# Kernel optimization log

Hardware: AMD Instinct MI355X
Metric: run time of the kernel (lower is better)

The kernel has to match this reference:

```python
import jax, jax.numpy as jnp
import numpy as np

N_NODES = 100000
N_EDGES = 600000
D = 128
N_TYPES = 3


def setup_inputs() -> dict:
    key = jax.random.key(0)
    ks = jax.random.split(key, 10)
    x = jax.random.normal(ks[0], (N_NODES, D), dtype=jnp.float32)
    edge_index = jax.random.randint(ks[1], (2, N_EDGES), 0, N_NODES, dtype=jnp.int64)
    edge_type_ids = jax.random.randint(ks[2], (N_EDGES,), 0, N_TYPES, dtype=jnp.int32)
    edge_weights = jax.random.uniform(ks[3], (N_EDGES,), dtype=jnp.float32)
    # Xavier-uniform linear weights (in==out==D), zero biases, uniform attention
    limit = float(np.sqrt(6.0 / (D + D)))
    W_edge = jax.random.uniform(ks[4], (N_TYPES, D, D), minval=-limit, maxval=limit, dtype=jnp.float32)
    b_edge = jnp.zeros((N_TYPES, D), dtype=jnp.float32)
    W_self = jax.random.uniform(ks[5], (D, D), minval=-limit, maxval=limit, dtype=jnp.float32)
    b_self = jnp.zeros((D,), dtype=jnp.float32)
    attention = jnp.ones((N_TYPES + 1,), dtype=jnp.float32) / (N_TYPES + 1)
    return {"x": x, "edge_index": edge_index, "edge_type_ids": edge_type_ids,
            "edge_weights": edge_weights, "W_edge": W_edge, "b_edge": b_edge,
            "W_self": W_self, "b_self": b_self, "attention": attention}


def reference(x, edge_index, edge_type_ids, edge_weights, W_edge, b_edge, W_self, b_self, attention):
    n_nodes = x.shape[0]
    n_types = W_edge.shape[0]
    src, dst = edge_index[0], edge_index[1]
    xs = x[src]  # (E, D) gather once, shared by all edge types
    outs = []
    for t in range(n_types):  # small fixed set of structurally distinct linears
        # mask zeros out edges of other types; equivalent to torch's boolean slicing
        m = jnp.where(edge_type_ids == t, edge_weights, jnp.zeros((), x.dtype))
        y = (xs @ W_edge[t] + b_edge[t]) * m[:, None]  # (E, D)
        outs.append(jax.ops.segment_sum(y, dst, num_segments=n_nodes))  # scatter-add
    outs.append(x @ W_self + b_self)
    stacked = jnp.stack(outs, axis=-1)  # (N, D, n_types+1)
    attn = jax.nn.softmax(attention)
    out = jnp.sum(stacked * attn, axis=-1)
    return jax.nn.gelu(out, approximate=False)  # torch F.gelu default is erf-based
```

## Files before the change

kernel.cpp:

```cpp
#include <hip/hip_runtime.h>
#include <hip/hip_bf16.h>
#include <math.h>

#define D 128
#define NT 3
#define KTOT (D * (NT + 1))
#define TM 32

typedef __attribute__((ext_vector_type(8))) __bf16 bf16x8;
typedef __attribute__((ext_vector_type(4))) float f32x4;

__device__ inline unsigned short f2bf(float f) {
    unsigned int u = __float_as_uint(f);
    unsigned int r = (u + 0x7FFFu + ((u >> 16) & 1u)) >> 16;
    return (unsigned short)r;
}
__device__ inline float bf2f(unsigned int hi16_as_low) {
    return __uint_as_float(hi16_as_low << 16);
}

__global__ void zero_kernel(float* __restrict__ p, long long n4) {
    long long i = (long long)blockIdx.x * blockDim.x + threadIdx.x;
    long long stride = (long long)gridDim.x * blockDim.x;
    float4 z = make_float4(0.f, 0.f, 0.f, 0.f);
    for (; i < n4; i += stride) ((float4*)p)[i] = z;
}

__global__ void prep_kernel(const float* __restrict__ W_edge, const float* __restrict__ b_edge,
                            const float* __restrict__ W_self, const float* __restrict__ b_self,
                            const float* __restrict__ attention,
                            float* __restrict__ wcat, float* __restrict__ biasb,
                            unsigned short* __restrict__ bfrag,
                            int* __restrict__ deg, int degN) {
    float a0 = attention[0], a1 = attention[1], a2 = attention[2], a3 = attention[3];
    float m = fmaxf(fmaxf(a0, a1), fmaxf(a2, a3));
    float e0 = expf(a0 - m), e1 = expf(a1 - m), e2 = expf(a2 - m), e3 = expf(a3 - m);
    float inv = 1.f / (e0 + e1 + e2 + e3);
    float at[4] = {e0 * inv, e1 * inv, e2 * inv, e3 * inv};

    int idx0 = blockIdx.x * blockDim.x + threadIdx.x;
    int stride = gridDim.x * blockDim.x;
    if (deg) {
        for (int i = idx0; i < degN; i += stride) deg[i] = 0;
    }
    for (int i = idx0; i < KTOT * D; i += stride) {
        int k = i >> 7, j = i & (D - 1);
        float v;
        if (k < D) {
            v = at[NT] * W_self[k * D + j];
        } else {
            int t = (k - D) >> 7;
            int kk = (k - D) & (D - 1);
            v = at[t] * W_edge[(t * D + kk) * D + j];
        }
        wcat[i] = v;
    }
    for (int i = idx0; i < KTOT; i += stride) {
        if (i < NT * D) {
            int t = i >> 7, j = i & (D - 1);
            biasb[i] = at[t] * b_edge[t * D + j];
        } else {
            biasb[i] = at[NT] * b_self[i - NT * D];
        }
    }
    if (bfrag) {
        for (int i = idx0; i < 16 * 8 * 64; i += stride) {
            int l = i & 63;
            int cf = (i >> 6) & 7;
            int step = i >> 9;
            int col = cf * 16 + (l & 15);
            int kb = step * 32 + ((l >> 4) * 8);
#pragma unroll
            for (int j = 0; j < 8; ++j) {
                int k = kb + j;
                float v;
                if (k < D) {
                    v = at[NT] * W_self[k * D + col];
                } else {
                    int t = (k - D) >> 7;
                    int kk = (k - D) & (D - 1);
                    v = at[t] * W_edge[(t * D + kk) * D + col];
                }
                bfrag[(size_t)i * 8 + j] = f2bf(v);
            }
        }
    }
}

__global__ __launch_bounds__(256) void fill_kernel(
    const int* __restrict__ ei, const int* __restrict__ et, const float* __restrict__ ew,
    int* __restrict__ deg, int2* __restrict__ csr, int* __restrict__ ovfcnt,
    int* __restrict__ ovflist, int nE, int cap) {
    int e = blockIdx.x * blockDim.x + threadIdx.x;
    if (e >= nE) return;
    int dst = ei[nE + e];
    int pos = atomicAdd(deg + dst, 1);
    if (pos < cap) {
        int src = ei[e];
        int t = et[e];
        csr[(size_t)dst * cap + pos] = make_int2(src | (t << 20), __float_as_int(ew[e]));
    } else {
        int o = atomicAdd(ovfcnt, 1);
        ovflist[o] = e;
    }
}

__global__ __launch_bounds__(512, 6) void fused_gemm_kernel(
    const float* __restrict__ x, const int2* __restrict__ csr, const int* __restrict__ deg,
    const unsigned short* __restrict__ bfrag, const float* __restrict__ biasb,
    const int* __restrict__ ei, const int* __restrict__ et, const float* __restrict__ ew,
    const int* __restrict__ ovfc, const int* __restrict__ ovfl,
    float* __restrict__ out, int nN, int nE, int cap) {
    __shared__ unsigned char lds[49536];
    float* sL = (float*)(lds + 49152);
    int t = threadIdx.x;
    int w = t >> 6;
    int lane = t & 63;
    int gl = lane & 15;
    int gbase = lane & 48;
    int row0 = blockIdx.x * TM;

#define BSTAGE(buf, st_) do {                                                                     \
        const unsigned short* gsrc = bfrag + (size_t)(st_) * 4096 + w * 512 + lane * 8;           \
        unsigned char* ldst = lds + 32768 + (buf) * 8192 + w * 1024;                              \
        __builtin_amdgcn_global_load_lds((const __attribute__((address_space(1))) void*)gsrc,     \
                                         (__attribute__((address_space(3))) void*)ldst, 16, 0, 0);\
    } while (0)

    BSTAGE(0, 0);

    int lrow = w * 4 + (lane >> 4);
    int node = row0 + lrow;
    int nclamp = (node < nN) ? node : (nN - 1);
    int dg = (node < nN) ? deg[nclamp] : 0;
    if (dg > cap) dg = cap;
    const int2* c = csr + (size_t)nclamp * cap;
    int2 mA = (gl < dg) ? c[gl] : make_int2(0, 0);
    int2 mB = (gl + 16 < dg) ? c[gl + 16] : make_int2(0, 0);

    float ac0[8], ac1[8], ac2[8];
#pragma unroll
    for (int j = 0; j < 8; ++j) { ac0[j] = 0.f; ac1[j] = 0.f; ac2[j] = 0.f; }
    float sw0 = 0.f, sw1 = 0.f, sw2 = 0.f;

    for (int i = 0; i < dg; i += 2) {
        int slA = gbase + (i & 15);
        int exA = __shfl((i < 16) ? mA.x : mB.x, slA);
        int ewA = __shfl((i < 16) ? mA.y : mB.y, slA);
        int srcA = exA & 0xFFFFF;
        if (srcA >= nN) srcA = 0;
        float wA = __int_as_float(ewA);
        int tA = (exA >> 20) & 3;
        bool actB = (i + 1 < dg);
        int slB = gbase + ((i + 1) & 15);
        int exB = __shfl((i + 1 < 16) ? mA.x : mB.x, slB);
        int ewB = __shfl((i + 1 < 16) ? mA.y : mB.y, slB);
        int srcB = exB & 0xFFFFF;
        if (!actB || srcB >= nN) srcB = 0;
        float wB = actB ? __int_as_float(ewB) : 0.f;
        int tB = (exB >> 20) & 3;

        const float* xsA = x + (size_t)srcA * D + gl * 8;
        const float* xsB = x + (size_t)srcB * D + gl * 8;
        float4 a0 = *(const float4*)(xsA);
        float4 a1 = *(const float4*)(xsA + 4);
        float4 b0 = *(const float4*)(xsB);
        float4 b1 = *(const float4*)(xsB + 4);

        float wA0 = (tA == 0) ? wA : 0.f;
        float wA1 = (tA == 1) ? wA : 0.f;
        float wA2 = (tA == 2) ? wA : 0.f;
        float wB0 = (tB == 0) ? wB : 0.f;
        float wB1 = (tB == 1) ? wB : 0.f;
        float wB2 = (tB == 2) ? wB : 0.f;
        sw0 += wA0 + wB0; sw1 += wA1 + wB1; sw2 += wA2 + wB2;

#define ACC4(v, j0, wt0, wt1, wt2)                                         \
        ac0[j0+0] = fmaf(wt0, v.x, ac0[j0+0]); ac0[j0+1] = fmaf(wt0, v.y, ac0[j0+1]); \
        ac0[j0+2] = fmaf(wt0, v.z, ac0[j0+2]); ac0[j0+3] = fmaf(wt0, v.w, ac0[j0+3]); \
        ac1[j0+0] = fmaf(wt1, v.x, ac1[j0+0]); ac1[j0+1] = fmaf(wt1, v.y, ac1[j0+1]); \
        ac1[j0+2] = fmaf(wt1, v.z, ac1[j0+2]); ac1[j0+3] = fmaf(wt1, v.w, ac1[j0+3]); \
        ac2[j0+0] = fmaf(wt2, v.x, ac2[j0+0]); ac2[j0+1] = fmaf(wt2, v.y, ac2[j0+1]); \
        ac2[j0+2] = fmaf(wt2, v.z, ac2[j0+2]); ac2[j0+3] = fmaf(wt2, v.w, ac2[j0+3]);
        ACC4(a0, 0, wA0, wA1, wA2)
        ACC4(a1, 4, wA0, wA1, wA2)
        ACC4(b0, 0, wB0, wB1, wB2)
        ACC4(b1, 4, wB0, wB1, wB2)
#undef ACC4
    }

    {
        int swz = lrow & 15;
        const float* xo = x + (size_t)nclamp * D + gl * 8;
        float4 v0 = *(const float4*)(xo);
        float4 v1 = *(const float4*)(xo + 4);
        uint4 o;
        o.x = (unsigned int)f2bf(v0.x) | ((unsigned int)f2bf(v0.y) << 16);
        o.y = (unsigned int)f2bf(v0.z) | ((unsigned int)f2bf(v0.w) << 16);
        o.z = (unsigned int)f2bf(v1.x) | ((unsigned int)f2bf(v1.y) << 16);
        o.w = (unsigned int)f2bf(v1.z) | ((unsigned int)f2bf(v1.w) << 16);
        *(uint4*)(lds + lrow * 1024 + ((gl ^ swz) << 4)) = o;
#define PACKST(arr, tt)                                                                \
        o.x = (unsigned int)f2bf(arr[0]) | ((unsigned int)f2bf(arr[1]) << 16);         \
        o.y = (unsigned int)f2bf(arr[2]) | ((unsigned int)f2bf(arr[3]) << 16);         \
        o.z = (unsigned int)f2bf(arr[4]) | ((unsigned int)f2bf(arr[5]) << 16);         \
        o.w = (unsigned int)f2bf(arr[6]) | ((unsigned int)f2bf(arr[7]) << 16);         \
        *(uint4*)(lds + lrow * 1024 + 256 + (tt) * 256 + ((gl ^ swz) << 4)) = o;
        PACKST(ac0, 0)
        PACKST(ac1, 1)
        PACKST(ac2, 2)
#undef PACKST
        if (gl < 3) {
            float sv = (gl == 0) ? sw0 : ((gl == 1) ? sw1 : sw2);
            sL[lrow * NT + gl] = sv;
        }
    }
    __syncthreads();

    int cnt = *ovfc;
    if (cnt > 0) {
        if (w == 0 && lane < 16) {
            for (int i = 0; i < cnt; ++i) {
                int e = ovfl[i];
                int dst = ei[nE + e];
                if (dst >= row0 && dst < row0 + TM && dst < nN) {
                    int tt = et[e];
                    float wt = ew[e];
                    int src = ei[e];
                    int lr = dst - row0;
                    int swz = lr & 15;
                    uint4* p = (uint4*)(lds + lr * 1024 + 256 + tt * 256 + ((lane ^ swz) << 4));
                    uint4 cu = *p;
                    const float* xs = x + (size_t)src * D + lane * 8;
                    float4 q0 = *(const float4*)(xs);
                    float4 q1 = *(const float4*)(xs + 4);
                    float f[8];
                    f[0] = bf2f(cu.x & 0xFFFF) + wt * q0.x; f[1] = bf2f(cu.x >> 16) + wt * q0.y;
                    f[2] = bf2f(cu.y & 0xFFFF) + wt * q0.z; f[3] = bf2f(cu.y >> 16) + wt * q0.w;
                    f[4] = bf2f(cu.z & 0xFFFF) + wt * q1.x; f[5] = bf2f(cu.z >> 16) + wt * q1.y;
                    f[6] = bf2f(cu.w & 0xFFFF) + wt * q1.z; f[7] = bf2f(cu.w >> 16) + wt * q1.w;
                    cu.x = (unsigned int)f2bf(f[0]) | ((unsigned int)f2bf(f[1]) << 16);
                    cu.y = (unsigned int)f2bf(f[2]) | ((unsigned int)f2bf(f[3]) << 16);
                    cu.z = (unsigned int)f2bf(f[4]) | ((unsigned int)f2bf(f[5]) << 16);
                    cu.w = (unsigned int)f2bf(f[6]) | ((unsigned int)f2bf(f[7]) << 16);
                    *p = cu;
                    if (lane == 0) sL[lr * NT + tt] += wt;
                }
            }
        }
        __syncthreads();
    }

    int ll = lane & 15;
    int ck = lane >> 4;
    f32x4 acc0 = (f32x4){0.f, 0.f, 0.f, 0.f};
    f32x4 acc1 = (f32x4){0.f, 0.f, 0.f, 0.f};
#pragma unroll 2
    for (int st = 0; st < 16; ++st) {
        int cur = st & 1;
        if (st < 15) BSTAGE(cur ^ 1, st + 1);
        int cc = st * 4 + ck;
        int phys = (cc & 48) | ((cc & 15) ^ ll);
        bf16x8 a0 = *(const bf16x8*)(lds + ll * 1024 + (phys << 4));
        bf16x8 a1 = *(const bf16x8*)(lds + (16 + ll) * 1024 + (phys << 4));
        bf16x8 b = *(const bf16x8*)(lds + 32768 + cur * 8192 + ((w * 64 + lane) << 4));
        acc0 = __builtin_amdgcn_mfma_f32_16x16x32_bf16(a0, b, acc0, 0, 0, 0);
        acc1 = __builtin_amdgcn_mfma_f32_16x16x32_bf16(a1, b, acc1, 0, 0, 0);
        __syncthreads();
    }
#undef BSTAGE

    int colb = w * 16 + ll;
    float bb0 = biasb[colb], bb1 = biasb[D + colb], bb2 = biasb[2 * D + colb], bs4 = biasb[3 * D + colb];
    const float kInvSqrt2 = 0.70710678118654752440f;
#pragma unroll
    for (int fr = 0; fr < 2; ++fr) {
        f32x4 A = fr ? acc1 : acc0;
#pragma unroll
        for (int reg = 0; reg < 4; ++reg) {
            int lr = fr * 16 + ck * 4 + reg;
            long row = (long)row0 + lr;
            if (row >= nN) continue;
            float s0 = sL[lr * NT + 0];
            float s1 = sL[lr * NT + 1];
            float s2 = sL[lr * NT + 2];
            float v = A[reg] + bs4 + s0 * bb0 + s1 * bb1 + s2 * bb2;
            v = 0.5f * v * (1.f + erff(v * kInvSqrt2));
            out[row * D + colb] = v;
        }
    }
}

__global__ __launch_bounds__(256) void scatterA_kernel(
    const float* __restrict__ x, const int* __restrict__ ei,
    const int* __restrict__ et, const float* __restrict__ ew,
    float* __restrict__ agg, float* __restrict__ s, int nE) {
    int gtid = blockIdx.x * blockDim.x + threadIdx.x;
    int wave = gtid >> 6;
    int lane = threadIdx.x & 63;
    int nw = (gridDim.x * blockDim.x) >> 6;
    for (int e = wave; e < nE; e += nw) {
        int src = ei[e];
        int dst = ei[nE + e];
        int t = et[e];
        float w = ew[e];
        float2 xv = *(const float2*)(x + (size_t)src * D + lane * 2);
        float* p = agg + (size_t)dst * (NT * D) + t * D + lane * 2;
        unsafeAtomicAdd(p, w * xv.x);
        unsafeAtomicAdd(p + 1, w * xv.y);
        if (lane == 0) unsafeAtomicAdd(s + (size_t)dst * NT + t, w);
    }
}

#define BM 64
#define BK 32
__global__ __launch_bounds__(256) void gemm_gelu_kernel(
    const float* __restrict__ x, const float* __restrict__ agg,
    const float* __restrict__ s, const float* __restrict__ wcat,
    const float* __restrict__ biasb, float* __restrict__ out, int nNodes) {
    __shared__ float As[BK][BM + 1];
    __shared__ float Bs[BK][D];

    int tx = threadIdx.x;
    int row0 = blockIdx.x * BM;
    int cg = tx & 31;
    int rg = tx >> 5;
    int lr = tx >> 3;
    int lc = (tx & 7) * 4;

    float acc[8][4];
#pragma unroll
    for (int i = 0; i < 8; ++i)
#pragma unroll
        for (int j = 0; j < 4; ++j) acc[i][j] = 0.f;

    for (int k0 = 0; k0 < KTOT; k0 += BK) {
        const float* srcBase;
        int strideA, koff;
        if (k0 < D) { srcBase = x; strideA = D; koff = k0; }
        else        { srcBase = agg; strideA = NT * D; koff = k0 - D; }
#pragma unroll
        for (int h = 0; h < 2; ++h) {
            int r = lr + h * 32;
            int node = row0 + r;
            if (node >= nNodes) node = nNodes - 1;
            float4 v = *(const float4*)(srcBase + (size_t)node * strideA + koff + lc);
            As[lc + 0][r] = v.x; As[lc + 1][r] = v.y;
            As[lc + 2][r] = v.z; As[lc + 3][r] = v.w;
        }
        {
            int br = tx >> 5;
            int bc = (tx & 31) * 4;
#pragma unroll
            for (int h = 0; h < 4; ++h) {
                int r = br + h * 8;
                *(float4*)(&Bs[r][bc]) = *(const float4*)(wcat + (size_t)(k0 + r) * D + bc);
            }
        }
        __syncthreads();
#pragma unroll
        for (int kk = 0; kk < BK; ++kk) {
            float4 b = *(const float4*)(&Bs[kk][cg * 4]);
            float a[8];
            *(float4*)(a)     = *(const float4*)(&As[kk][rg * 8]);
            *(float4*)(a + 4) = *(const float4*)(&As[kk][rg * 8 + 4]);
#pragma unroll
            for (int i = 0; i < 8; ++i) {
                acc[i][0] = fmaf(a[i], b.x, acc[i][0]);
                acc[i][1] = fmaf(a[i], b.y, acc[i][1]);
                acc[i][2] = fmaf(a[i], b.z, acc[i][2]);
                acc[i][3] = fmaf(a[i], b.w, acc[i][3]);
            }
        }
        __syncthreads();
    }

    int jc = cg * 4;
    float4 bb0 = *(const float4*)(biasb + 0 * D + jc);
    float4 bb1 = *(const float4*)(biasb + 1 * D + jc);
    float4 bb2 = *(const float4*)(biasb + 2 * D + jc);
    float4 bsv = *(const float4*)(biasb + NT * D + jc);
#pragma unroll
    for (int i = 0; i < 8; ++i) {
        int node = row0 + rg * 8 + i;
        if (node >= nNodes) break;
        float s0 = s[(size_t)node * NT + 0];
        float s1 = s[(size_t)node * NT + 1];
        float s2 = s[(size_t)node * NT + 2];
        float4 r;
        r.x = acc[i][0] + bsv.x + s0 * bb0.x + s1 * bb1.x + s2 * bb2.x;
        r.y = acc[i][1] + bsv.y + s0 * bb0.y + s1 * bb1.y + s2 * bb2.y;
        r.z = acc[i][2] + bsv.z + s0 * bb0.z + s1 * bb1.z + s2 * bb2.z;
        r.w = acc[i][3] + bsv.w + s0 * bb0.w + s1 * bb1.w + s2 * bb2.w;
        const float kInvSqrt2 = 0.70710678118654752440f;
        r.x = 0.5f * r.x * (1.f + erff(r.x * kInvSqrt2));
        r.y = 0.5f * r.y * (1.f + erff(r.y * kInvSqrt2));
        r.z = 0.5f * r.z * (1.f + erff(r.z * kInvSqrt2));
        r.w = 0.5f * r.w * (1.f + erff(r.w * kInvSqrt2));
        *(float4*)(out + (size_t)node * D + jc) = r;
    }
}

__global__ __launch_bounds__(256) void selfmv_kernel(
    const float* __restrict__ x, const float* __restrict__ Ws,
    const float* __restrict__ bs, const float* __restrict__ attn,
    float* __restrict__ out, int nN) {
    float a0 = attn[0], a1 = attn[1], a2 = attn[2], a3 = attn[3];
    float m = fmaxf(fmaxf(a0, a1), fmaxf(a2, a3));
    float e3 = expf(a3 - m);
    float inv = 1.f / (expf(a0 - m) + expf(a1 - m) + expf(a2 - m) + e3);
    float at3 = e3 * inv;
    int wave = (blockIdx.x * blockDim.x + threadIdx.x) >> 6;
    int lane = threadIdx.x & 63;
    int nw = (gridDim.x * blockDim.x) >> 6;
    for (int n = wave; n < nN; n += nw) {
        float2 xr = *(const float2*)(x + (size_t)n * D + lane * 2);
        float acc0 = 0.f, acc1 = 0.f;
#pragma unroll
        for (int k = 0; k < D; ++k) {
            float xv = __shfl((k & 1) ? xr.y : xr.x, k >> 1);
            float2 wv = *(const float2*)(Ws + (size_t)k * D + lane * 2);
            acc0 = fmaf(xv, wv.x, acc0);
            acc1 = fmaf(xv, wv.y, acc1);
        }
        float2 r;
        r.x = at3 * (acc0 + bs[lane * 2]);
        r.y = at3 * (acc1 + bs[lane * 2 + 1]);
        *(float2*)(out + (size_t)n * D + lane * 2) = r;
    }
}

__global__ __launch_bounds__(256) void edgemv_kernel(
    const float* __restrict__ x, const int* __restrict__ ei,
    const int* __restrict__ et, const float* __restrict__ ew,
    const float* __restrict__ We, const float* __restrict__ be,
    const float* __restrict__ attn, float* __restrict__ out, int nE) {
    float a0 = attn[0], a1 = attn[1], a2 = attn[2], a3 = attn[3];
    float m = fmaxf(fmaxf(a0, a1), fmaxf(a2, a3));
    float e0 = expf(a0 - m), e1 = expf(a1 - m), e2 = expf(a2 - m), e3 = expf(a3 - m);
    float inv = 1.f / (e0 + e1 + e2 + e3);
    float at[NT] = {e0 * inv, e1 * inv, e2 * inv};
    int wave = (blockIdx.x * blockDim.x + threadIdx.x) >> 6;
    int lane = threadIdx.x & 63;
    int nw = (gridDim.x * blockDim.x) >> 6;
    for (int e = wave; e < nE; e += nw) {
        int src = ei[e];
        int dst = ei[nE + e];
        int t = et[e];
        float sc = ew[e] * at[t];
        const float* W = We + (size_t)t * D * D;
        float2 xr = *(const float2*)(x + (size_t)src * D + lane * 2);
        float acc0 = 0.f, acc1 = 0.f;
#pragma unroll
        for (int k = 0; k < D; ++k) {
            float xv = __shfl((k & 1) ? xr.y : xr.x, k >> 1);
            float2 wv = *(const float2*)(W + (size_t)k * D + lane * 2);
            acc0 = fmaf(xv, wv.x, acc0);
            acc1 = fmaf(xv, wv.y, acc1);
        }
        float* p = out + (size_t)dst * D + lane * 2;
        unsafeAtomicAdd(p,     sc * (acc0 + be[(size_t)t * D + lane * 2]));
        unsafeAtomicAdd(p + 1, sc * (acc1 + be[(size_t)t * D + lane * 2 + 1]));
    }
}

__global__ void gelu_kernel(float* __restrict__ p, long long n4) {
    long long i = (long long)blockIdx.x * blockDim.x + threadIdx.x;
    long long stride = (long long)gridDim.x * blockDim.x;
    const float kInvSqrt2 = 0.70710678118654752440f;
    for (; i < n4; i += stride) {
        float4 r = ((float4*)p)[i];
        r.x = 0.5f * r.x * (1.f + erff(r.x * kInvSqrt2));
        r.y = 0.5f * r.y * (1.f + erff(r.y * kInvSqrt2));
        r.z = 0.5f * r.z * (1.f + erff(r.z * kInvSqrt2));
        r.w = 0.5f * r.w * (1.f + erff(r.w * kInvSqrt2));
        ((float4*)p)[i] = r;
    }
}

extern "C" void kernel_launch(void* const* d_in, const int* in_sizes, int n_in,
                              void* d_out, int out_size, void* d_ws, size_t ws_size,
                              hipStream_t stream) {
    const float* x = (const float*)d_in[0];
    const int* ei = (const int*)d_in[1];
    const int* et = (const int*)d_in[2];
    const float* ew = (const float*)d_in[3];
    const float* W_edge = (const float*)d_in[4];
    const float* b_edge = (const float*)d_in[5];
    const float* W_self = (const float*)d_in[6];
    const float* b_self = (const float*)d_in[7];
    const float* attention = (const float*)d_in[8];
    float* out = (float*)d_out;

    const int nN = in_sizes[0] / D;
    const int nE = in_sizes[2];
    const int cap = 32;

    size_t needFused = (size_t)(KTOT * D + KTOT) * 4 + 131072
                     + 4 * ((size_t)nN + 2 + (size_t)nE) + 8ull * nN * cap;

    if (ws_size >= needFused && nN < (1 << 20)) {
        float* wcat = (float*)d_ws;
        float* biasb = wcat + (size_t)KTOT * D;
        unsigned short* bfrag = (unsigned short*)(biasb + KTOT);
        int* deg = (int*)(bfrag + 65536);
        int* ovfc = deg + nN;
        int* ovfl = ovfc + 2;
        int2* csr = (int2*)(ovfl + nE);

        hipLaunchKernelGGL(prep_kernel, dim3(64), dim3(256), 0, stream,
                           W_edge, b_edge, W_self, b_self, attention, wcat, biasb, bfrag,
                           deg, nN + 2);
        hipLaunchKernelGGL(fill_kernel, dim3((nE + 255) / 256), dim3(256), 0, stream,
                           ei, et, ew, deg, csr, ovfc, ovfl, nE, cap);
        hipLaunchKernelGGL(fused_gemm_kernel, dim3((nN + TM - 1) / TM), dim3(512), 0, stream,
                           x, csr, deg, bfrag, biasb, ei, et, ew, ovfc, ovfl, out, nN, nE, cap);
        return;
    }

    const size_t baseFloats = (size_t)nN * NT * D + (size_t)nN * NT + (size_t)KTOT * D + KTOT;
    if (ws_size >= baseFloats * 4) {
        float* agg = (float*)d_ws;
        float* sW = agg + (size_t)nN * NT * D;
        float* wcat = sW + (size_t)nN * NT;
        float* biasb = wcat + (size_t)KTOT * D;
        long long zeroFloats = (long long)nN * (NT * D + NT);
        hipLaunchKernelGGL(zero_kernel, dim3(2048), dim3(256), 0, stream, agg, (zeroFloats + 3) / 4);
        hipLaunchKernelGGL(prep_kernel, dim3(64), dim3(256), 0, stream,
                           W_edge, b_edge, W_self, b_self, attention, wcat, biasb,
                           (unsigned short*)nullptr, (int*)nullptr, 0);
        hipLaunchKernelGGL(scatterA_kernel, dim3(2048), dim3(256), 0, stream,
                           x, ei, et, ew, agg, sW, nE);
        hipLaunchKernelGGL(gemm_gelu_kernel, dim3((nN + BM - 1) / BM), dim3(256), 0, stream,
                           x, agg, sW, wcat, biasb, out, nN);
    } else {
        hipLaunchKernelGGL(selfmv_kernel, dim3(2048), dim3(256), 0, stream,
                           x, W_self, b_self, attention, out, nN);
        hipLaunchKernelGGL(edgemv_kernel, dim3(2048), dim3(256), 0, stream,
                           x, ei, et, ew, W_edge, b_edge, attention, out, nE);
        hipLaunchKernelGGL(gelu_kernel, dim3(2048), dim3(256), 0, stream,
                           out, (long long)nN * D / 4);
    }
}
```

Measured before the change: 123.5 us.

## Bin edges per 32-node block and gather bf16 copy of x

Replaces the per-node CSR fill with per-block edge buckets (32 destination nodes per bucket), which are sorted into a per-row CSR in LDS inside the fused kernel. A combined kernel also converts x to bf16 once, so every neighbor gather reads half as many bytes. The intent is to cut global atomics and scattered CSR writes and to halve gather traffic. In exchange it adds an extra full pass writing xb, LDS atomics and a local overflow path, and neighbor features are rounded to bf16 before aggregation.

```diff
diff --git a/kernel.cpp b/kernel.cpp
--- a/kernel.cpp
+++ b/kernel.cpp
@@ -6,6 +6,8 @@
 #define NT 3
 #define KTOT (D * (NT + 1))
 #define TM 32
+#define BCAP 320
+#define NCAP 32
 
 typedef __attribute__((ext_vector_type(8))) __bf16 bf16x8;
 typedef __attribute__((ext_vector_type(4))) float f32x4;
@@ -15,8 +17,8 @@
     unsigned int r = (u + 0x7FFFu + ((u >> 16) & 1u)) >> 16;
     return (unsigned short)r;
 }
-__device__ inline float bf2f(unsigned int hi16_as_low) {
-    return __uint_as_float(hi16_as_low << 16);
+__device__ inline float bf2f(unsigned int low16) {
+    return __uint_as_float(low16 << 16);
 }
 
 __global__ void zero_kernel(float* __restrict__ p, long long n4) {
@@ -31,7 +33,7 @@
                             const float* __restrict__ attention,
                             float* __restrict__ wcat, float* __restrict__ biasb,
                             unsigned short* __restrict__ bfrag,
-                            int* __restrict__ deg, int degN) {
+                            int* __restrict__ zeroMe, int zeroN) {
     float a0 = attention[0], a1 = attention[1], a2 = attention[2], a3 = attention[3];
     float m = fmaxf(fmaxf(a0, a1), fmaxf(a2, a3));
     float e0 = expf(a0 - m), e1 = expf(a1 - m), e2 = expf(a2 - m), e3 = expf(a3 - m);
@@ -40,8 +42,8 @@
 
     int idx0 = blockIdx.x * blockDim.x + threadIdx.x;
     int stride = gridDim.x * blockDim.x;
-    if (deg) {
-        for (int i = idx0; i < degN; i += stride) deg[i] = 0;
+    if (zeroMe) {
+        for (int i = idx0; i < zeroN; i += stride) zeroMe[i] = 0;
     }
     for (int i = idx0; i < KTOT * D; i += stride) {
         int k = i >> 7, j = i & (D - 1);
@@ -87,37 +89,59 @@
     }
 }
 
-__global__ __launch_bounds__(256) void fill_kernel(
+__global__ __launch_bounds__(256) void xcvt_bin_kernel(
+    const float* __restrict__ x, unsigned short* __restrict__ xb, int nN,
     const int* __restrict__ ei, const int* __restrict__ et, const float* __restrict__ ew,
-    int* __restrict__ deg, int2* __restrict__ csr, int* __restrict__ ovfcnt,
-    int* __restrict__ ovflist, int nE, int cap) {
-    int e = blockIdx.x * blockDim.x + threadIdx.x;
-    if (e >= nE) return;
-    int dst = ei[nE + e];
-    int pos = atomicAdd(deg + dst, 1);
-    if (pos < cap) {
-        int src = ei[e];
-        int t = et[e];
-        csr[(size_t)dst * cap + pos] = make_int2(src | (t << 20), __float_as_int(ew[e]));
+    int* __restrict__ bcnt, int2* __restrict__ bucket,
+    int* __restrict__ ovfc, int* __restrict__ ovflist, int nE, int XB) {
+    int b = blockIdx.x;
+    if (b < XB) {
+        int i = b * 256 + threadIdx.x;
+        int total = nN * (D / 4);
+        int stride = XB * 256;
+        for (; i < total; i += stride) {
+            int n = i >> 5;
+            int c4 = (i & 31) * 4;
+            float4 v = *(const float4*)(x + (size_t)n * D + c4);
+            ushort4 o;
+            o.x = f2bf(v.x); o.y = f2bf(v.y); o.z = f2bf(v.z); o.w = f2bf(v.w);
+            *(ushort4*)(xb + (size_t)n * D + c4) = o;
+        }
     } else {
-        int o = atomicAdd(ovfcnt, 1);
-        ovflist[o] = e;
-    }
-}
-
-__global__ __launch_bounds__(512, 6) void fused_gemm_kernel(
-    const float* __restrict__ x, const int2* __restrict__ csr, const int* __restrict__ deg,
-    const unsigned short* __restrict__ bfrag, const float* __restrict__ biasb,
+        int e = (b - XB) * 256 + threadIdx.x;
+        if (e >= nE) return;
+        int dst = ei[nE + e];
+        int bu = dst >> 5;
+        int pos = atomicAdd(bcnt + bu, 1);
+        if (pos < BCAP) {
+            int src = ei[e];
+            int t = et[e];
+            bucket[(size_t)bu * BCAP + pos] =
+                make_int2(src | (t << 20) | ((dst & 31) << 22), __float_as_int(ew[e]));
+        } else {
+            int o = atomicAdd(ovfc, 1);
+            ovflist[o] = e;
+        }
+    }
+}
+
+__global__ __launch_bounds__(512, 4) void fusedB_kernel(
+    const unsigned short* __restrict__ xb, const int2* __restrict__ bucket,
+    const int* __restrict__ bcnt, const unsigned short* __restrict__ bfrag,
+    const float* __restrict__ biasb,
     const int* __restrict__ ei, const int* __restrict__ et, const float* __restrict__ ew,
-    const int* __restrict__ ovfc, const int* __restrict__ ovfl,
-    float* __restrict__ out, int nN, int nE, int cap) {
-    __shared__ unsigned char lds[49536];
+    const int* __restrict__ ovfc, const int* __restrict__ ovflist,
+    float* __restrict__ out, int nN, int nE) {
+    __shared__ unsigned char lds[60424];
     float* sL = (float*)(lds + 49152);
+    int2* lcsr = (int2*)(lds + 49536);
+    int* ldeg = (int*)(lds + 57728);
+    int2* lovf = (int2*)(lds + 57856);
+    int* lovfc = (int*)(lds + 60416);
+
     int t = threadIdx.x;
     int w = t >> 6;
     int lane = t & 63;
-    int gl = lane & 15;
-    int gbase = lane & 48;
     int row0 = blockIdx.x * TM;
 
 #define BSTAGE(buf, st_) do {                                                                     \
@@ -129,14 +153,30 @@
 
     BSTAGE(0, 0);
 
+    if (t < 32) ldeg[t] = 0;
+    if (t == 32) *lovfc = 0;
+    __syncthreads();
+
+    int cnt = bcnt[blockIdx.x];
+    if (cnt > BCAP) cnt = BCAP;
+    for (int i = t; i < cnt; i += 512) {
+        int2 eo = bucket[(size_t)blockIdx.x * BCAP + i];
+        int lr = (eo.x >> 22) & 31;
+        int pos = atomicAdd(&ldeg[lr], 1);
+        if (pos < NCAP) lcsr[lr * NCAP + pos] = eo;
+        else { int lp = atomicAdd(lovfc, 1); lovf[lp] = eo; }
+    }
+    __syncthreads();
+
+    int gl = lane & 15;
+    int gbase = lane & 48;
     int lrow = w * 4 + (lane >> 4);
     int node = row0 + lrow;
     int nclamp = (node < nN) ? node : (nN - 1);
-    int dg = (node < nN) ? deg[nclamp] : 0;
-    if (dg > cap) dg = cap;
-    const int2* c = csr + (size_t)nclamp * cap;
-    int2 mA = (gl < dg) ? c[gl] : make_int2(0, 0);
-    int2 mB = (gl + 16 < dg) ? c[gl + 16] : make_int2(0, 0);
+    int dg = ldeg[lrow];
+    if (dg > NCAP) dg = NCAP;
+    int2 mA = (gl < dg) ? lcsr[lrow * NCAP + gl] : make_int2(0, 0);
+    int2 mB = (gl + 16 < dg) ? lcsr[lrow * NCAP + gl + 16] : make_int2(0, 0);
 
     float ac0[8], ac1[8], ac2[8];
 #pragma unroll
@@ -160,12 +200,8 @@
         float wB = actB ? __int_as_float(ewB) : 0.f;
         int tB = (exB >> 20) & 3;
 
-        const float* xsA = x + (size_t)srcA * D + gl * 8;
-        const float* xsB = x + (size_t)srcB * D + gl * 8;
-        float4 a0 = *(const float4*)(xsA);
-        float4 a1 = *(const float4*)(xsA + 4);
-        float4 b0 = *(const float4*)(xsB);
-        float4 b1 = *(const float4*)(xsB + 4);
+        uint4 xa = *(const uint4*)(xb + (size_t)srcA * D + gl * 8);
+        uint4 xbv = *(const uint4*)(xb + (size_t)srcB * D + gl * 8);
 
         float wA0 = (tA == 0) ? wA : 0.f;
         float wA1 = (tA == 1) ? wA : 0.f;
@@ -175,31 +211,29 @@
         float wB2 = (tB == 2) ? wB : 0.f;
         sw0 += wA0 + wB0; sw1 += wA1 + wB1; sw2 += wA2 + wB2;
 
-#define ACC4(v, j0, wt0, wt1, wt2)                                         \
-        ac0[j0+0] = fmaf(wt0, v.x, ac0[j0+0]); ac0[j0+1] = fmaf(wt0, v.y, ac0[j0+1]); \
-        ac0[j0+2] = fmaf(wt0, v.z, ac0[j0+2]); ac0[j0+3] = fmaf(wt0, v.w, ac0[j0+3]); \
-        ac1[j0+0] = fmaf(wt1, v.x, ac1[j0+0]); ac1[j0+1] = fmaf(wt1, v.y, ac1[j0+1]); \
-        ac1[j0+2] = fmaf(wt1, v.z, ac1[j0+2]); ac1[j0+3] = fmaf(wt1, v.w, ac1[j0+3]); \
-        ac2[j0+0] = fmaf(wt2, v.x, ac2[j0+0]); ac2[j0+1] = fmaf(wt2, v.y, ac2[j0+1]); \
-        ac2[j0+2] = fmaf(wt2, v.z, ac2[j0+2]); ac2[j0+3] = fmaf(wt2, v.w, ac2[j0+3]);
-        ACC4(a0, 0, wA0, wA1, wA2)
-        ACC4(a1, 4, wA0, wA1, wA2)
-        ACC4(b0, 0, wB0, wB1, wB2)
-        ACC4(b1, 4, wB0, wB1, wB2)
-#undef ACC4
+        float f0, f1;
+#define ACCUM(u, j0, j1, w0_, w1_, w2_)                                   \
+        f0 = __uint_as_float((u) << 16);                                  \
+        f1 = __uint_as_float((u) & 0xFFFF0000u);                          \
+        ac0[j0] = fmaf(w0_, f0, ac0[j0]); ac0[j1] = fmaf(w0_, f1, ac0[j1]); \
+        ac1[j0] = fmaf(w1_, f0, ac1[j0]); ac1[j1] = fmaf(w1_, f1, ac1[j1]); \
+        ac2[j0] = fmaf(w2_, f0, ac2[j0]); ac2[j1] = fmaf(w2_, f1, ac2[j1]);
+        ACCUM(xa.x, 0, 1, wA0, wA1, wA2)
+        ACCUM(xa.y, 2, 3, wA0, wA1, wA2)
+        ACCUM(xa.z, 4, 5, wA0, wA1, wA2)
+        ACCUM(xa.w, 6, 7, wA0, wA1, wA2)
+        ACCUM(xbv.x, 0, 1, wB0, wB1, wB2)
+        ACCUM(xbv.y, 2, 3, wB0, wB1, wB2)
+        ACCUM(xbv.z, 4, 5, wB0, wB1, wB2)
+        ACCUM(xbv.w, 6, 7, wB0, wB1, wB2)
+#undef ACCUM
     }
 
     {
         int swz = lrow & 15;
-        const float* xo = x + (size_t)nclamp * D + gl * 8;
-        float4 v0 = *(const float4*)(xo);
-        float4 v1 = *(const float4*)(xo + 4);
+        uint4 xo = *(const uint4*)(xb + (size_t)nclamp * D + gl * 8);
+        *(uint4*)(lds + lrow * 1024 + ((gl ^ swz) << 4)) = xo;
         uint4 o;
-        o.x = (unsigned int)f2bf(v0.x) | ((unsigned int)f2bf(v0.y) << 16);
-        o.y = (unsigned int)f2bf(v0.z) | ((unsigned int)f2bf(v0.w) << 16);
-        o.z = (unsigned int)f2bf(v1.x) | ((unsigned int)f2bf(v1.y) << 16);
-        o.w = (unsigned int)f2bf(v1.z) | ((unsigned int)f2bf(v1.w) << 16);
-        *(uint4*)(lds + lrow * 1024 + ((gl ^ swz) << 4)) = o;
 #define PACKST(arr, tt)                                                                \
         o.x = (unsigned int)f2bf(arr[0]) | ((unsigned int)f2bf(arr[1]) << 16);         \
         o.y = (unsigned int)f2bf(arr[2]) | ((unsigned int)f2bf(arr[3]) << 16);         \
@@ -217,32 +251,57 @@
     }
     __syncthreads();
 
-    int cnt = *ovfc;
-    if (cnt > 0) {
+    int lcnt = *lovfc;
+    int gcnt = *ovfc;
+    if (lcnt > 0 || gcnt > 0) {
         if (w == 0 && lane < 16) {
-            for (int i = 0; i < cnt; ++i) {
-                int e = ovfl[i];
+            for (int i = 0; i < lcnt; ++i) {
+                int2 eo = lovf[i];
+                int lr = (eo.x >> 22) & 31;
+                int tt = (eo.x >> 20) & 3;
+                int src = eo.x & 0xFFFFF;
+                float wt = __int_as_float(eo.y);
+                uint4* p = (uint4*)(lds + lr * 1024 + 256 + tt * 256 + ((lane ^ (lr & 15)) << 4));
+                uint4 cu = *p;
+                uint4 xr = *(const uint4*)(xb + (size_t)src * D + lane * 8);
+                float f0 = bf2f(cu.x & 0xFFFF) + wt * bf2f(xr.x & 0xFFFF);
+                float f1 = bf2f(cu.x >> 16)    + wt * bf2f(xr.x >> 16);
+                float f2 = bf2f(cu.y & 0xFFFF) + wt * bf2f(xr.y & 0xFFFF);
+                float f3 = bf2f(cu.y >> 16)    + wt * bf2f(xr.y >> 16);
+                float f4 = bf2f(cu.z & 0xFFFF) + wt * bf2f(xr.z & 0xFFFF);
+                float f5 = bf2f(cu.z >> 16)    + wt * bf2f(xr.z >> 16);
+                float f6 = bf2f(cu.w & 0xFFFF) + wt * bf2f(xr.w & 0xFFFF);
+                float f7 = bf2f(cu.w >> 16)    + wt * bf2f(xr.w >> 16);
+                cu.x = (unsigned int)f2bf(f0) | ((unsigned int)f2bf(f1) << 16);
+                cu.y = (unsigned int)f2bf(f2) | ((unsigned int)f2bf(f3) << 16);
+                cu.z = (unsigned int)f2bf(f4) | ((unsigned int)f2bf(f5) << 16);
+                cu.w = (unsigned int)f2bf(f6) | ((unsigned int)f2bf(f7) << 16);
+                *p = cu;
+                if (lane == 0) sL[lr * NT + tt] += wt;
+            }
+            for (int i = 0; i < gcnt; ++i) {
+                int e = ovflist[i];
                 int dst = ei[nE + e];
                 if (dst >= row0 && dst < row0 + TM && dst < nN) {
                     int tt = et[e];
                     float wt = ew[e];
                     int src = ei[e];
                     int lr = dst - row0;
-                    int swz = lr & 15;
-                    uint4* p = (uint4*)(lds + lr * 1024 + 256 + tt * 256 + ((lane ^ swz) << 4));
+                    uint4* p = (uint4*)(lds + lr * 1024 + 256 + tt * 256 + ((lane ^ (lr & 15)) << 4));
                     uint4 cu = *p;
-                    const float* xs = x + (size_t)src * D + lane * 8;
-                    float4 q0 = *(const float4*)(xs);
-                    float4 q1 = *(const float4*)(xs + 4);
-                    float f[8];
-                    f[0] = bf2f(cu.x & 0xFFFF) + wt * q0.x; f[1] = bf2f(cu.x >> 16) + wt * q0.y;
-                    f[2] = bf2f(cu.y & 0xFFFF) + wt * q0.z; f[3] = bf2f(cu.y >> 16) + wt * q0.w;
-                    f[4] = bf2f(cu.z & 0xFFFF) + wt * q1.x; f[5] = bf2f(cu.z >> 16) + wt * q1.y;
-                    f[6] = bf2f(cu.w & 0xFFFF) + wt * q1.z; f[7] = bf2f(cu.w >> 16) + wt * q1.w;
-                    cu.x = (unsigned int)f2bf(f[0]) | ((unsigned int)f2bf(f[1]) << 16);
-                    cu.y = (unsigned int)f2bf(f[2]) | ((unsigned int)f2bf(f[3]) << 16);
-                    cu.z = (unsigned int)f2bf(f[4]) | ((unsigned int)f2bf(f[5]) << 16);
-                    cu.w = (unsigned int)f2bf(f[6]) | ((unsigned int)f2bf(f[7]) << 16);
+                    uint4 xr = *(const uint4*)(xb + (size_t)src * D + lane * 8);
+                    float f0 = bf2f(cu.x & 0xFFFF) + wt * bf2f(xr.x & 0xFFFF);
+                    float f1 = bf2f(cu.x >> 16)    + wt * bf2f(xr.x >> 16);
+                    float f2 = bf2f(cu.y & 0xFFFF) + wt * bf2f(xr.y & 0xFFFF);
+                    float f3 = bf2f(cu.y >> 16)    + wt * bf2f(xr.y >> 16);
+                    float f4 = bf2f(cu.z & 0xFFFF) + wt * bf2f(xr.z & 0xFFFF);
+                    float f5 = bf2f(cu.z >> 16)    + wt * bf2f(xr.z >> 16);
+                    float f6 = bf2f(cu.w & 0xFFFF) + wt * bf2f(xr.w & 0xFFFF);
+                    float f7 = bf2f(cu.w >> 16)    + wt * bf2f(xr.w >> 16);
+                    cu.x = (unsigned int)f2bf(f0) | ((unsigned int)f2bf(f1) << 16);
+                    cu.y = (unsigned int)f2bf(f2) | ((unsigned int)f2bf(f3) << 16);
+                    cu.z = (unsigned int)f2bf(f4) | ((unsigned int)f2bf(f5) << 16);
+                    cu.w = (unsigned int)f2bf(f6) | ((unsigned int)f2bf(f7) << 16);
                     *p = cu;
                     if (lane == 0) sL[lr * NT + tt] += wt;
                 }
@@ -494,27 +553,39 @@
 
     const int nN = in_sizes[0] / D;
     const int nE = in_sizes[2];
-    const int cap = 32;
-
-    size_t needFused = (size_t)(KTOT * D + KTOT) * 4 + 131072
-                     + 4 * ((size_t)nN + 2 + (size_t)nE) + 8ull * nN * cap;
+    const int nb = (nN + TM - 1) / TM;
+
+    size_t off = 0;
+    auto take = [&](size_t bytes) { size_t o = (off + 15) & ~(size_t)15; off = o + bytes; return o; };
+    size_t o_wcat  = take((size_t)KTOT * D * 4);
+    size_t o_biasb = take((size_t)KTOT * 4);
+    size_t o_bfrag = take(131072);
+    size_t o_bcnt  = take((size_t)(nb + 2) * 4);
+    size_t o_ovfl  = take((size_t)nE * 4);
+    size_t o_buck  = take((size_t)nb * BCAP * 8);
+    size_t o_xb    = take((size_t)nN * D * 2);
+    size_t needFused = off;
 
     if (ws_size >= needFused && nN < (1 << 20)) {
-        float* wcat = (float*)d_ws;
-        float* biasb = wcat + (size_t)KTOT * D;
-        unsigned short* bfrag = (unsigned short*)(biasb + KTOT);
-        int* deg = (int*)(bfrag + 65536);
-        int* ovfc = deg + nN;
-        int* ovfl = ovfc + 2;
-        int2* csr = (int2*)(ovfl + nE);
+        char* ws = (char*)d_ws;
+        float* wcat = (float*)(ws + o_wcat);
+        float* biasb = (float*)(ws + o_biasb);
+        unsigned short* bfrag = (unsigned short*)(ws + o_bfrag);
+        int* bcnt = (int*)(ws + o_bcnt);
+        int* ovfc = bcnt + nb;
+        int* ovfl = (int*)(ws + o_ovfl);
+        int2* bucket = (int2*)(ws + o_buck);
+        unsigned short* xb = (unsigned short*)(ws + o_xb);
 
         hipLaunchKernelGGL(prep_kernel, dim3(64), dim3(256), 0, stream,
                            W_edge, b_edge, W_self, b_self, attention, wcat, biasb, bfrag,
-                           deg, nN + 2);
-        hipLaunchKernelGGL(fill_kernel, dim3((nE + 255) / 256), dim3(256), 0, stream,
-                           ei, et, ew, deg, csr, ovfc, ovfl, nE, cap);
-        hipLaunchKernelGGL(fused_gemm_kernel, dim3((nN + TM - 1) / TM), dim3(512), 0, stream,
-                           x, csr, deg, bfrag, biasb, ei, et, ew, ovfc, ovfl, out, nN, nE, cap);
+                           bcnt, nb + 2);
+        const int XB = 512;
+        const int FB = (nE + 255) / 256;
+        hipLaunchKernelGGL(xcvt_bin_kernel, dim3(XB + FB), dim3(256), 0, stream,
+                           x, xb, nN, ei, et, ew, bcnt, bucket, ovfc, ovfl, nE, XB);
+        hipLaunchKernelGGL(fusedB_kernel, dim3(nb), dim3(512), 0, stream,
+                           xb, bucket, bcnt, bfrag, biasb, ei, et, ew, ovfc, ovfl, out, nN, nE);
         return;
     }
 
```

After: 167.8 us. +35.9%, slower.
